# Kernel tuning notes

Measured on AMD Instinct MI355X. Metric: run time of the kernel, lower is better.

Reference implementation:

```python
import jax, jax.numpy as jnp
import numpy as np

NUM_HEADS = 8
EMBED_DIM = 512
EXPAND = 3
RPE_DIM = 512
RPE_LAYERS = 3
B, N = 4, 2048
D1 = (EXPAND * EMBED_DIM) // NUM_HEADS * NUM_HEADS  # 1536
HEAD_DIM = D1 // NUM_HEADS  # 192


def srms(x):
    # SimpleRMSNorm: x / (||x||_2 * d^{-1/2} + eps)
    d = x.shape[-1]
    rms = jnp.linalg.norm(x, axis=-1, keepdims=True) * (d ** -0.5)
    return x / (rms + 1e-8)


def rpe_net(idx, Wp, bp, Wl, bl, Wr, br):
    # idx: (m, 1) relative positions -> (m, h*head_dim)
    h = idx @ Wp.T + bp
    for i in range(Wl.shape[0]):  # fixed small layer count
        h = jax.nn.relu(srms(h)) @ Wl[i].T + bl[i]
    return jax.nn.relu(srms(h)) @ Wr.T + br


def setup_inputs() -> dict:
    key = jax.random.key(0)
    ks = jax.random.split(key, 12)
    s = 0.02
    return {
        "x": jax.random.normal(ks[0], (B, N, EMBED_DIM), jnp.float32),
        "Wu": jax.random.normal(ks[1], (D1, EMBED_DIM), jnp.float32) * s,
        "bu": jnp.zeros((D1,), jnp.float32),
        "Wv": jax.random.normal(ks[2], (D1, EMBED_DIM), jnp.float32) * s,
        "bv": jnp.zeros((D1,), jnp.float32),
        "Wo": jax.random.normal(ks[3], (EMBED_DIM, D1), jnp.float32) * s,
        "bo": jnp.zeros((EMBED_DIM,), jnp.float32),
        "Wp": jax.random.normal(ks[4], (RPE_DIM, 1), jnp.float32) * s,
        "bp": jax.random.normal(ks[5], (RPE_DIM,), jnp.float32) * s,
        "Wl": jax.random.normal(ks[6], (RPE_LAYERS, RPE_DIM, RPE_DIM), jnp.float32) * s,
        "bl": jax.random.normal(ks[7], (RPE_LAYERS, RPE_DIM), jnp.float32) * s,
        "Wr": jax.random.normal(ks[8], (NUM_HEADS * HEAD_DIM, RPE_DIM), jnp.float32) * s,
        "br": jax.random.normal(ks[9], (NUM_HEADS * HEAD_DIM,), jnp.float32) * s,
    }


def reference(x, Wu, bu, Wv, bv, Wo, bo, Wp, bp, Wl, bl, Wr, br):
    b, n, e = x.shape
    d1 = Wu.shape[0]
    hd = d1 // NUM_HEADS
    u = jax.nn.silu(x @ Wu.T + bu)                       # (b, n, d1)
    v = jax.nn.silu(x @ Wv.T + bv)                       # (b, n, d1)
    v = v.reshape(b, n, NUM_HEADS, hd).transpose(0, 2, 1, 3)  # (b, h, n, d)
    # Tno non-causal, par_type=1: indices [0, 1..n-1, 0, -(n-1)..-1]
    pos = jnp.arange(1, n, dtype=x.dtype)
    zero = jnp.zeros((1,), x.dtype)
    idx = jnp.concatenate([zero, pos, zero, -pos[::-1]])[:, None]  # (2n, 1)
    a = rpe_net(idx, Wp, bp, Wl, bl, Wr, br)             # (2n, h*d)
    a = a.reshape(2 * n, NUM_HEADS, hd).transpose(1, 0, 2)  # (h, 2n, d)
    m = 2 * n
    # circular conv of length 2n along sequence, truncate to n
    y = jnp.fft.rfft(v, m, axis=2) * jnp.fft.rfft(a, m, axis=1)[None]
    out = jnp.fft.irfft(y, m, axis=2)[:, :, :n, :]       # (b, h, n, d)
    out = out.transpose(0, 2, 1, 3).reshape(b, n, d1)    # (b, n, d1)
    return (u * out) @ Wo.T + bo
```

## Files before the change

kernel.cpp:

```cpp
#include <hip/hip_runtime.h>

#define N_SEQ 2048
#define M_FFT 4096
#define D1    1536
#define NH    8
#define HD    192
#define ED    512

typedef __bf16 bf16;
typedef __bf16 bf16x2 __attribute__((ext_vector_type(2)));
typedef __bf16 bf16x4 __attribute__((ext_vector_type(4)));
typedef __bf16 bf16x8 __attribute__((ext_vector_type(8)));
typedef float  floatx4 __attribute__((ext_vector_type(4)));

enum { MODE_PLAIN = 0, MODE_SILU_UV = 1, MODE_AT = 3 };

__device__ __forceinline__ void gload16(const void* g, void* l) {
    __builtin_amdgcn_global_load_lds(
        (const __attribute__((address_space(1))) void*)g,
        (__attribute__((address_space(3))) void*)l, 16, 0, 0);
}

template<int MODE, typename OutT>
__global__ __launch_bounds__(256) void gemm_bf16(
    const bf16* __restrict__ A, const bf16* __restrict__ Bw,
    const float* __restrict__ bias, const float* __restrict__ bias2,
    OutT* __restrict__ C, OutT* __restrict__ C2,
    int M, int Nc, int K)
{
    __shared__ __align__(16) bf16 As[128 * 32];
    __shared__ __align__(16) bf16 Bs[128 * 32];

    const int tid  = threadIdx.x;
    const int row0 = blockIdx.y * 128;
    const int col0 = blockIdx.x * 128;
    const int wid  = tid >> 6;
    const int lane = tid & 63;
    const int lm   = lane & 15;
    const int lk   = lane >> 4;
    const int wm   = wid >> 1;
    const int wn   = wid & 1;
    const int ldrow  = tid >> 2;
    const int ldcol8 = (tid & 3) * 8;

    floatx4 acc[4][4] = {};

    const bf16* Ag = A  + ((size_t)(row0 + ldrow)) * K + ldcol8;
    const bf16* Bg = Bw + ((size_t)(col0 + ldrow)) * K + ldcol8;
    bf16* AsW = As + (wid * 16) * 32;
    bf16* BsW = Bs + (wid * 16) * 32;

    for (int k0 = 0; k0 < K; k0 += 32) {
        gload16(Ag + k0, AsW);
        gload16(Ag + (size_t)64 * K + k0, AsW + 64 * 32);
        gload16(Bg + k0, BsW);
        gload16(Bg + (size_t)64 * K + k0, BsW + 64 * 32);
        __syncthreads();

        bf16x8 af[4], bfr[4];
        #pragma unroll
        for (int mi = 0; mi < 4; ++mi)
            af[mi] = *(const bf16x8*)&As[(wm * 64 + mi * 16 + lm) * 32 + lk * 8];
        #pragma unroll
        for (int nj = 0; nj < 4; ++nj)
            bfr[nj] = *(const bf16x8*)&Bs[(wn * 64 + nj * 16 + lm) * 32 + lk * 8];
        #pragma unroll
        for (int mi = 0; mi < 4; ++mi)
            #pragma unroll
            for (int nj = 0; nj < 4; ++nj)
                acc[mi][nj] = __builtin_amdgcn_mfma_f32_16x16x32_bf16(
                    af[mi], bfr[nj], acc[mi][nj], 0, 0, 0);
        __syncthreads();
    }

    const float* bs = bias;
    OutT* dst = C;
    int cadj = 0;
    if (MODE == MODE_SILU_UV && col0 >= D1) { bs = bias2; dst = C2; cadj = D1; }

    float bcol[4];
    #pragma unroll
    for (int nj = 0; nj < 4; ++nj)
        bcol[nj] = bs[col0 - cadj + wn * 64 + nj * 16 + lm];

    #pragma unroll
    for (int mi = 0; mi < 4; ++mi) {
        const int rbase = row0 + wm * 64 + mi * 16 + lk * 4;
        #pragma unroll
        for (int nj = 0; nj < 4; ++nj) {
            const int col = col0 - cadj + wn * 64 + nj * 16 + lm;
            float vals[4];
            #pragma unroll
            for (int r = 0; r < 4; ++r) {
                float val = acc[mi][nj][r] + bcol[nj];
                if (MODE == MODE_SILU_UV)
                    val = val / (1.0f + __expf(-val));
                vals[r] = val;
            }
            if (MODE == MODE_SILU_UV) {
                int b = rbase >> 11, s = rbase & 2047;
                bf16x4 o;
                #pragma unroll
                for (int r = 0; r < 4; ++r) o[r] = (bf16)vals[r];
                *(bf16x4*)&((bf16*)dst)[((size_t)(b * D1 + col)) * N_SEQ + s] = o;
            } else if (MODE == MODE_AT) {
                float4 o = make_float4(vals[0], vals[1], vals[2], vals[3]);
                *(float4*)&((float*)C)[(size_t)col * M + rbase] = o;
            } else {
                #pragma unroll
                for (int r = 0; r < 4; ++r)
                    C[(size_t)(rbase + r) * Nc + col] = (OutT)vals[r];
            }
        }
    }
}

__global__ __launch_bounds__(256) void f2b_all_kernel(
    const float* __restrict__ x,  const float* __restrict__ s0,
    const float* __restrict__ s1, const float* __restrict__ s2,
    const float* __restrict__ s3, const float* __restrict__ s4,
    bf16* __restrict__ x_bf, bf16* __restrict__ w_bf)
{
    const int bid = blockIdx.x;
    const float* src;
    bf16* dst;
    size_t off;
    if (bid < 4096) {
        src = x; dst = x_bf; off = (size_t)bid * 1024;
    } else {
        int t = bid - 4096;
        int seg = t / 768;
        src = seg == 0 ? s0 : seg == 1 ? s1 : seg == 2 ? s2 : seg == 3 ? s3 : s4;
        dst = w_bf + (size_t)seg * 786432;
        off = (size_t)(t % 768) * 1024;
    }
    size_t i = off + (size_t)threadIdx.x * 4;
    float4 f = *(const float4*)(src + i);
    union { bf16 h[4]; short4 s; } u4;
    u4.h[0] = (bf16)f.x; u4.h[1] = (bf16)f.y;
    u4.h[2] = (bf16)f.z; u4.h[3] = (bf16)f.w;
    *(short4*)(dst + i) = u4.s;
}

__global__ __launch_bounds__(256) void rpe_in_srms_kernel(
    const float* __restrict__ Wp, const float* __restrict__ bp,
    bf16* __restrict__ g)
{
    const int j = blockIdx.x;
    const int tid = threadIdx.x;
    float idxv = (j < N_SEQ) ? (float)j
                             : (j == N_SEQ ? 0.0f : (float)(j - 2 * N_SEQ));
    float h1 = idxv * Wp[tid] + bp[tid];
    float h2 = idxv * Wp[tid + 256] + bp[tid + 256];
    float ss = h1 * h1 + h2 * h2;
    #pragma unroll
    for (int off = 32; off > 0; off >>= 1) ss += __shfl_down(ss, off, 64);
    __shared__ float red[4];
    if ((tid & 63) == 0) red[tid >> 6] = ss;
    __syncthreads();
    float tot = red[0] + red[1] + red[2] + red[3];
    float scale = 1.0f / (sqrtf(tot) * 0.04419417382415922f + 1e-8f);
    g[(size_t)j * ED + tid]       = (bf16)fmaxf(h1 * scale, 0.0f);
    g[(size_t)j * ED + tid + 256] = (bf16)fmaxf(h2 * scale, 0.0f);
}

__global__ __launch_bounds__(256) void srms_relu_kernel(
    const float* __restrict__ in, bf16* __restrict__ out)
{
    const int row = blockIdx.x;
    const int tid = threadIdx.x;
    const float* p = in + (size_t)row * ED;

    float ss = 0.0f;
    for (int i = tid; i < ED; i += 256) { float x = p[i]; ss += x * x; }
    #pragma unroll
    for (int off = 32; off > 0; off >>= 1) ss += __shfl_down(ss, off, 64);
    __shared__ float red[4];
    if ((tid & 63) == 0) red[tid >> 6] = ss;
    __syncthreads();
    float tot = red[0] + red[1] + red[2] + red[3];
    float scale = 1.0f / (sqrtf(tot) * 0.04419417382415922f + 1e-8f);
    for (int i = tid; i < ED; i += 256)
        out[(size_t)row * ED + i] = (bf16)fmaxf(p[i] * scale, 0.0f);
}

#define FFT_LDS_SZ 4381
#define CC1 0.9238795325112867f
#define SS1 0.3826834323650898f
#define RR2 0.7071067811865476f

__device__ __forceinline__ int fpad(int i) { return i + (i >> 4) + 2 * (i >> 8); }

__device__ __forceinline__ float2 cmul(float2 a, float2 b) {
    return make_float2(a.x * b.x - a.y * b.y, a.x * b.y + a.y * b.x);
}
__device__ __forceinline__ float2 cadd(float2 a, float2 b) {
    return make_float2(a.x + b.x, a.y + b.y);
}
__device__ __forceinline__ float2 csub(float2 a, float2 b) {
    return make_float2(a.x - b.x, a.y - b.y);
}
__device__ __forceinline__ float2 cneg_i(float2 a) { return make_float2(a.y, -a.x); }
__device__ __forceinline__ float2 cpos_i(float2 a) { return make_float2(-a.y, a.x); }
__host__ __device__ constexpr int brev4(int t) {
    return ((t & 1) << 3) | ((t & 2) << 1) | ((t & 4) >> 1) | ((t & 8) >> 3);
}

template<bool HZ>
__device__ __forceinline__ void fft16_dif_r4(float2 x[16]) {
    const float2 W1 = make_float2( CC1, -SS1);
    const float2 W2 = make_float2( RR2, -RR2);
    const float2 W3 = make_float2( SS1, -CC1);
    const float2 W6 = make_float2(-RR2, -RR2);
    const float2 W9 = make_float2(-CC1,  SS1);
    #pragma unroll
    for (int n = 0; n < 4; ++n) {
        float2 A, B, C, D;
        if (HZ) { A = x[n]; C = x[n]; B = x[n + 4]; D = x[n + 4]; }
        else {
            A = cadd(x[n], x[n + 8]);  C = csub(x[n], x[n + 8]);
            B = cadd(x[n + 4], x[n + 12]); D = csub(x[n + 4], x[n + 12]);
        }
        float2 s = csub(A, B);
        float2 nid = cneg_i(D);
        float2 m = cadd(C, nid);
        float2 p = csub(C, nid);
        x[n] = cadd(A, B);
        if (n == 0)      { x[4] = s;            x[8]  = m;           x[12] = p; }
        else if (n == 1) { x[5] = cmul(s, W2);  x[9]  = cmul(m, W1); x[13] = cmul(p, W3); }
        else if (n == 2) { x[6] = cneg_i(s);    x[10] = cmul(m, W2); x[14] = cmul(p, W6); }
        else             { x[7] = cmul(s, W6);  x[11] = cmul(m, W3); x[15] = cmul(p, W9); }
    }
    #pragma unroll
    for (int q = 0; q < 16; q += 4) {
        float2 a = x[q], b = x[q + 1], c = x[q + 2], d = x[q + 3];
        float2 a1 = cadd(a, c), c1 = csub(a, c);
        float2 b1 = cadd(b, d), d1 = cneg_i(csub(b, d));
        x[q]     = cadd(a1, b1);
        x[q + 1] = csub(a1, b1);
        x[q + 2] = cadd(c1, d1);
        x[q + 3] = csub(c1, d1);
    }
}

template<bool HALF_OUT>
__device__ __forceinline__ void fft16_dit_inv_r4(float2 x[16]) {
    const float2 V1 = make_float2( CC1, SS1);
    const float2 V2 = make_float2( RR2, RR2);
    const float2 V3 = make_float2( SS1, CC1);
    const float2 V6 = make_float2(-RR2, RR2);
    #pragma unroll
    for (int q = 0; q < 16; q += 4) {
        float2 a = x[q], b = x[q + 1], c = x[q + 2], d = x[q + 3];
        float2 a1 = cadd(a, b), b1 = csub(a, b);
        float2 c1 = cadd(c, d), d1 = csub(c, d);
        float2 t = cpos_i(d1);
        x[q]     = cadd(a1, c1);
        x[q + 2] = csub(a1, c1);
        x[q + 1] = cadd(b1, t);
        x[q + 3] = csub(b1, t);
    }
    #pragma unroll
    for (int n = 0; n < 4; ++n) {
        float2 t1, t2;
        if (n == 0)      { t1 = x[4];             t2 = x[12]; }
        else if (n == 1) { t1 = cmul(x[5],  V2);  t2 = cmul(x[13], V2); }
        else if (n == 2) { t1 = cpos_i(x[6]);     t2 = cpos_i(x[14]); }
        else             { t1 = cmul(x[7],  V6);  t2 = cmul(x[15], V6); }
        float2 P = cadd(x[n], t1), Q = csub(x[n], t1);
        float2 R = cadd(x[n + 8], t2), S = csub(x[n + 8], t2);
        float2 t, u;
        if (n == 0)      { t = R;            u = S; }
        else if (n == 1) { t = cmul(R, V1);  u = cmul(S, V1); }
        else if (n == 2) { t = cmul(R, V2);  u = cmul(S, V2); }
        else             { t = cmul(R, V3);  u = cmul(S, V3); }
        float2 iu = cpos_i(u);
        x[n]     = cadd(P, t);
        x[n + 4] = cadd(Q, iu);
        if (!HALF_OUT) {
            x[n + 8]  = csub(P, t);
            x[n + 12] = csub(Q, iu);
        }
    }
}

__device__ __forceinline__ void stage_twiddle_tree(
    float2 v[16], int j, float rden, float sgn)
{
    float s, c;
    __sincosf(sgn * 6.283185307179586f * (float)j * rden, &s, &c);
    float2 w[16];
    w[1] = make_float2(c, s);
    w[2] = cmul(w[1], w[1]);
    w[3] = cmul(w[1], w[2]);
    w[4] = cmul(w[2], w[2]);
    w[5] = cmul(w[1], w[4]);
    w[6] = cmul(w[2], w[4]);
    w[7] = cmul(w[3], w[4]);
    w[8] = cmul(w[4], w[4]);
    #pragma unroll
    for (int t = 9; t < 16; ++t) w[t] = cmul(w[t - 8], w[8]);
    #pragma unroll
    for (int tau = 1; tau < 16; ++tau)
        v[brev4(tau)] = cmul(v[brev4(tau)], w[tau]);
}

template<bool HALF_ZERO>
__device__ void fft4096_fwd(float2* d, int tid)
{
    float2 v[16];
    {
        const int j = tid;
        if (HALF_ZERO) {
            #pragma unroll
            for (int t = 0; t < 8; ++t) v[t] = d[fpad(j + (t << 8))];
            fft16_dif_r4<true>(v);
        } else {
            #pragma unroll
            for (int t = 0; t < 16; ++t) v[t] = d[fpad(j + (t << 8))];
            fft16_dif_r4<false>(v);
        }
        stage_twiddle_tree(v, j, 1.0f / 4096.0f, -1.0f);
        #pragma unroll
        for (int p = 0; p < 16; ++p) d[fpad(j + (p << 8))] = v[p];
    }
    __syncthreads();
    {
        const int base = ((tid >> 4) << 8) + (tid & 15);
        #pragma unroll
        for (int t = 0; t < 16; ++t) v[t] = d[fpad(base + (t << 4))];
        fft16_dif_r4<false>(v);
        stage_twiddle_tree(v, tid & 15, 1.0f / 256.0f, -1.0f);
        #pragma unroll
        for (int p = 0; p < 16; ++p) d[fpad(base + (p << 4))] = v[p];
    }
    __syncthreads();
    {
        const int base = tid << 4;
        #pragma unroll
        for (int t = 0; t < 16; ++t) v[t] = d[fpad(base + t)];
        fft16_dif_r4<false>(v);
        #pragma unroll
        for (int p = 0; p < 16; ++p) d[fpad(base + p)] = v[p];
    }
    __syncthreads();
}

__global__ __launch_bounds__(256) void fft_a_kernel(
    const float* __restrict__ a_t, float2* __restrict__ Wspec)
{
    __shared__ float2 data[FFT_LDS_SZ];
    const int tid = threadIdx.x;
    const int h = blockIdx.x / 96, dp = blockIdx.x % 96;

    const float* r0 = a_t + ((size_t)(h * HD + 2 * dp)) * M_FFT;
    const float* r1 = r0 + M_FFT;

    for (int j = tid; j < 4096; j += 256) data[fpad(j)] = make_float2(r0[j], r1[j]);
    __syncthreads();
    fft4096_fwd<false>(data, tid);

    float2* outrow = Wspec + (size_t)blockIdx.x * 4096;
    for (int j = tid; j < 4096; j += 256) outrow[j] = data[fpad(j)];
}

__global__ __launch_bounds__(256) void fft_conv_kernel(
    const bf16* __restrict__ v_t, const float2* __restrict__ Wspec,
    const bf16* __restrict__ u_t, bf16* __restrict__ gated_t)
{
    __shared__ float2 data[FFT_LDS_SZ];
    const int tid = threadIdx.x;
    const int bx = blockIdx.x;
    const int b  = bx / 768;
    const int r  = bx % 768;
    const int h  = r / 96, dp = r % 96;
    const int ch = h * HD + 2 * dp;

    const bf16* z0 = v_t + ((size_t)(b * D1 + ch)) * N_SEQ;
    const bf16* z1 = z0 + N_SEQ;

    {
        const int s = tid * 8;
        bf16x8 a0 = *(const bf16x8*)(z0 + s);
        bf16x8 a1 = *(const bf16x8*)(z1 + s);
        #pragma unroll
        for (int i = 0; i < 8; ++i)
            data[fpad(s + i)] = make_float2((float)a0[i], (float)a1[i]);
    }
    __syncthreads();

    fft4096_fwd<true>(data, tid);

    const float2* Wrow = Wspec + (size_t)r * 4096;
    float2 v[16];
    {
        const int base = tid << 4;
        #pragma unroll
        for (int i = 0; i < 16; ++i) {
            const int p  = base + i;
            const int k  = __brev((unsigned)p) >> 20;
            const int km = (4096 - k) & 4095;
            const int p2 = __brev((unsigned)km) >> 20;
            float2 Zk = data[fpad(p)];
            float2 Zm = data[fpad(p2)];
            float2 Wk = Wrow[p];
            float2 Wm = Wrow[p2];
            float2 V0 = make_float2(0.5f * (Zk.x + Zm.x), 0.5f * (Zk.y - Zm.y));
            float2 V1 = make_float2(0.5f * (Zk.y + Zm.y), 0.5f * (Zm.x - Zk.x));
            float2 A0 = make_float2(0.5f * (Wk.x + Wm.x), 0.5f * (Wk.y - Wm.y));
            float2 A1 = make_float2(0.5f * (Wk.y + Wm.y), 0.5f * (Wm.x - Wk.x));
            float2 P = cmul(V0, A0), Q = cmul(V1, A1);
            v[i] = make_float2(P.x - Q.y, P.y + Q.x);
        }
        __syncthreads();
        fft16_dit_inv_r4<false>(v);
        #pragma unroll
        for (int i = 0; i < 16; ++i) data[fpad(base + i)] = v[i];
    }
    __syncthreads();
    {
        const int base = ((tid >> 4) << 8) + (tid & 15);
        #pragma unroll
        for (int p = 0; p < 16; ++p) v[p] = data[fpad(base + (p << 4))];
        stage_twiddle_tree(v, tid & 15, 1.0f / 256.0f, 1.0f);
        fft16_dit_inv_r4<false>(v);
        #pragma unroll
        for (int t = 0; t < 16; ++t) data[fpad(base + (t << 4))] = v[t];
    }
    __syncthreads();
    {
        const int j = tid;
        #pragma unroll
        for (int p = 0; p < 16; ++p) v[p] = data[fpad(j + (p << 8))];
        stage_twiddle_tree(v, j, 1.0f / 4096.0f, 1.0f);
        fft16_dit_inv_r4<true>(v);
        #pragma unroll
        for (int t = 0; t < 8; ++t) data[fpad(j + (t << 8))] = v[t];
    }
    __syncthreads();

    const float inv_m = 1.0f / 4096.0f;
    const bf16* u0 = u_t + ((size_t)(b * D1 + ch)) * N_SEQ;
    const bf16* u1 = u0 + N_SEQ;
    bf16* g0 = gated_t + ((size_t)(b * D1 + ch)) * N_SEQ;
    bf16* g1 = g0 + N_SEQ;
    {
        const int t = tid * 8;
        bf16x8 ua = *(const bf16x8*)(u0 + t);
        bf16x8 ub = *(const bf16x8*)(u1 + t);
        bf16x8 oa, ob;
        #pragma unroll
        for (int i = 0; i < 8; ++i) {
            float2 y = data[fpad(t + i)];
            oa[i] = (bf16)(y.x * inv_m * (float)ua[i]);
            ob[i] = (bf16)(y.y * inv_m * (float)ub[i]);
        }
        *(bf16x8*)(g0 + t) = oa;
        *(bf16x8*)(g1 + t) = ob;
    }
}

__global__ __launch_bounds__(256) void transpose_cs_kernel(
    const bf16* __restrict__ in, bf16* __restrict__ outp)
{
    __shared__ bf16 tile[64 * 68];
    const int c0 = blockIdx.x * 64;
    const int m0 = blockIdx.y * 64;
    const int b  = m0 >> 11;
    const int s0 = m0 & 2047;
    const int tid = threadIdx.x;
    const int cl = tid >> 4;
    const int sc = (tid & 15) * 4;
    #pragma unroll
    for (int p = 0; p < 4; ++p) {
        int c = p * 16 + cl;
        bf16x4 v = *(const bf16x4*)&in[((size_t)(b * D1 + c0 + c)) * N_SEQ + s0 + sc];
        *(bf16x4*)&tile[c * 68 + sc] = v;
    }
    __syncthreads();
    const int sl = tid >> 4;
    const int cc = (tid & 15) * 4;
    #pragma unroll
    for (int p = 0; p < 4; ++p) {
        int s = p * 16 + sl;
        bf16x4 o;
        #pragma unroll
        for (int j = 0; j < 4; ++j) o[j] = tile[(cc + j) * 68 + s];
        *(bf16x4*)&outp[((size_t)(m0 + s)) * D1 + c0 + cc] = o;
    }
}

extern "C" void kernel_launch(void* const* d_in, const int* in_sizes, int n_in,
                              void* d_out, int out_size, void* d_ws, size_t ws_size,
                              hipStream_t stream)
{
    const float* x  = (const float*)d_in[0];
    const float* Wu = (const float*)d_in[1];
    const float* bu = (const float*)d_in[2];
    const float* Wv = (const float*)d_in[3];
    const float* bv = (const float*)d_in[4];
    const float* Wo = (const float*)d_in[5];
    const float* bo = (const float*)d_in[6];
    const float* Wp = (const float*)d_in[7];
    const float* bp = (const float*)d_in[8];
    const float* Wl = (const float*)d_in[9];
    const float* bl = (const float*)d_in[10];
    const float* Wr = (const float*)d_in[11];
    const float* br = (const float*)d_in[12];
    float* out = (float*)d_out;

    float* ws      = (float*)d_ws;
    float* a_t     = ws;
    float* Wspec   = a_t   + 6291456;
    float* h0      = Wspec + 6291456;
    bf16*  bfws    = (bf16*)(h0 + 2097152);
    bf16*  x_bf    = bfws;
    bf16*  w_bf    = x_bf    + 4194304;
    bf16*  Wuv_bf  = w_bf;
    bf16*  Wo_bf   = w_bf    + 2 * 786432;
    bf16*  Wl_bf   = Wo_bf   + 786432;
    bf16*  Wr_bf   = Wl_bf   + 786432;
    bf16*  g_bf    = Wr_bf   + 786432;
    bf16*  u_t     = g_bf    + 2097152;
    bf16*  v_t     = u_t     + 12582912;
    bf16*  gated_t = v_t     + 12582912;
    bf16*  gated   = gated_t + 12582912;

    dim3 blk(256);

    f2b_all_kernel<<<4096 + 5 * 768, blk, 0, stream>>>(
        x, Wu, Wv, Wo, Wl, Wr, x_bf, w_bf);

    gemm_bf16<MODE_SILU_UV, bf16><<<dim3(24, 64), blk, 0, stream>>>(
        x_bf, Wuv_bf, bu, bv, u_t, v_t, 8192, 2 * D1, ED);

    rpe_in_srms_kernel<<<4096, blk, 0, stream>>>(Wp, bp, g_bf);
    for (int i = 0; i < 3; ++i) {
        gemm_bf16<MODE_PLAIN, float><<<dim3(4, 32), blk, 0, stream>>>(
            g_bf, Wl_bf + (size_t)i * ED * ED, bl + (size_t)i * ED, nullptr,
            h0, nullptr, 4096, ED, ED);
        srms_relu_kernel<<<4096, blk, 0, stream>>>(h0, g_bf);
    }
    gemm_bf16<MODE_AT, float><<<dim3(12, 32), blk, 0, stream>>>(
        g_bf, Wr_bf, br, nullptr, a_t, nullptr, 4096, D1, ED);

    fft_a_kernel<<<768, blk, 0, stream>>>(a_t, (float2*)Wspec);
    fft_conv_kernel<<<3072, blk, 0, stream>>>(
        v_t, (const float2*)Wspec, u_t, gated_t);

    transpose_cs_kernel<<<dim3(24, 128), blk, 0, stream>>>(gated_t, gated);

    gemm_bf16<MODE_PLAIN, float><<<dim3(4, 64), blk, 0, stream>>>(
        gated, Wo_bf, bo, nullptr, out, nullptr, 8192, ED, D1);
}
```

Before: 365.5 us.

## Fuse RPE SimpleRMSNorm into GEMM epilogues via atomic row sum-of-squares

The standalone srms_relu kernels and the fp32 intermediate h0 are removed. Each RPE layer GEMM now stores relu of the unnormalized output as bf16 and atomically accumulates per-row sums of squares. Since the norm scale is positive, the next GEMM applies it to its accumulators in the epilogue, and the AT GEMM does the same for the last layer. The RPE input kernel and the sumsq zeroing are folded into the f2b conversion launch, and the FFT complex type becomes a float2 ext_vector so the compiler can use packed math. This cuts several launches and an fp32 round trip, at the cost of float atomics and scalar bf16 stores in the epilogue.

Result: no change. 358.8 us (-1.8%).

```diff
diff --git a/kernel.cpp b/kernel.cpp
--- a/kernel.cpp
+++ b/kernel.cpp
@@ -8,12 +8,12 @@
 #define ED    512
 
 typedef __bf16 bf16;
-typedef __bf16 bf16x2 __attribute__((ext_vector_type(2)));
 typedef __bf16 bf16x4 __attribute__((ext_vector_type(4)));
 typedef __bf16 bf16x8 __attribute__((ext_vector_type(8)));
 typedef float  floatx4 __attribute__((ext_vector_type(4)));
-
-enum { MODE_PLAIN = 0, MODE_SILU_UV = 1, MODE_AT = 3 };
+typedef float  cx __attribute__((ext_vector_type(2)));
+
+enum { MODE_PLAIN = 0, MODE_SILU_UV = 1, MODE_AT = 3, MODE_RPE = 4 };
 
 __device__ __forceinline__ void gload16(const void* g, void* l) {
     __builtin_amdgcn_global_load_lds(
@@ -26,7 +26,8 @@
     const bf16* __restrict__ A, const bf16* __restrict__ Bw,
     const float* __restrict__ bias, const float* __restrict__ bias2,
     OutT* __restrict__ C, OutT* __restrict__ C2,
-    int M, int Nc, int K)
+    int M, int Nc, int K,
+    const float* __restrict__ scale_in, float* __restrict__ sumsq_out)
 {
     __shared__ __align__(16) bf16 As[128 * 32];
     __shared__ __align__(16) bf16 Bs[128 * 32];
@@ -83,16 +84,50 @@
     for (int nj = 0; nj < 4; ++nj)
         bcol[nj] = bs[col0 - cadj + wn * 64 + nj * 16 + lm];
 
+    if (MODE == MODE_RPE) {
+        #pragma unroll
+        for (int mi = 0; mi < 4; ++mi) {
+            #pragma unroll
+            for (int r = 0; r < 4; ++r) {
+                const int row = row0 + wm * 64 + mi * 16 + lk * 4 + r;
+                float sc = 1.0f;
+                if (scale_in)
+                    sc = 1.0f / (sqrtf(scale_in[row]) * 0.04419417382415922f + 1e-8f);
+                float ssq = 0.0f;
+                #pragma unroll
+                for (int nj = 0; nj < 4; ++nj) {
+                    const int col = col0 + wn * 64 + nj * 16 + lm;
+                    float val = acc[mi][nj][r] * sc + bcol[nj];
+                    ssq += val * val;
+                    ((bf16*)C)[(size_t)row * Nc + col] = (bf16)fmaxf(val, 0.0f);
+                }
+                ssq += __shfl_xor(ssq, 1, 64);
+                ssq += __shfl_xor(ssq, 2, 64);
+                ssq += __shfl_xor(ssq, 4, 64);
+                ssq += __shfl_xor(ssq, 8, 64);
+                if (lm == 0) atomicAdd(&sumsq_out[row], ssq);
+            }
+        }
+        return;
+    }
+
     #pragma unroll
     for (int mi = 0; mi < 4; ++mi) {
         const int rbase = row0 + wm * 64 + mi * 16 + lk * 4;
+        float sc[4];
+        #pragma unroll
+        for (int r = 0; r < 4; ++r) {
+            sc[r] = 1.0f;
+            if (MODE == MODE_AT && scale_in)
+                sc[r] = 1.0f / (sqrtf(scale_in[rbase + r]) * 0.04419417382415922f + 1e-8f);
+        }
         #pragma unroll
         for (int nj = 0; nj < 4; ++nj) {
             const int col = col0 - cadj + wn * 64 + nj * 16 + lm;
             float vals[4];
             #pragma unroll
             for (int r = 0; r < 4; ++r) {
-                float val = acc[mi][nj][r] + bcol[nj];
+                float val = acc[mi][nj][r] * sc[r] + bcol[nj];
                 if (MODE == MODE_SILU_UV)
                     val = val / (1.0f + __expf(-val));
                 vals[r] = val;
@@ -119,69 +154,53 @@
     const float* __restrict__ x,  const float* __restrict__ s0,
     const float* __restrict__ s1, const float* __restrict__ s2,
     const float* __restrict__ s3, const float* __restrict__ s4,
-    bf16* __restrict__ x_bf, bf16* __restrict__ w_bf)
+    const float* __restrict__ Wp, const float* __restrict__ bp,
+    bf16* __restrict__ x_bf, bf16* __restrict__ w_bf,
+    float* __restrict__ sumsq, bf16* __restrict__ g0)
 {
     const int bid = blockIdx.x;
-    const float* src;
-    bf16* dst;
-    size_t off;
-    if (bid < 4096) {
-        src = x; dst = x_bf; off = (size_t)bid * 1024;
+    const int tid = threadIdx.x;
+    __shared__ float red[4];
+
+    if (bid < 7936) {
+        const float* src;
+        bf16* dst;
+        size_t off;
+        if (bid < 4096) {
+            src = x; dst = x_bf; off = (size_t)bid * 1024;
+        } else {
+            int t = bid - 4096;
+            int seg = t / 768;
+            src = seg == 0 ? s0 : seg == 1 ? s1 : seg == 2 ? s2
+                : seg == 3 ? s3 : s4;
+            dst = w_bf + (size_t)seg * 786432;
+            off = (size_t)(t % 768) * 1024;
+        }
+        size_t i = off + (size_t)tid * 4;
+        float4 f = *(const float4*)(src + i);
+        union { bf16 h[4]; short4 s; } u4;
+        u4.h[0] = (bf16)f.x; u4.h[1] = (bf16)f.y;
+        u4.h[2] = (bf16)f.z; u4.h[3] = (bf16)f.w;
+        *(short4*)(dst + i) = u4.s;
+    } else if (bid < 7948) {
+        size_t i = (size_t)(bid - 7936) * 1024 + (size_t)tid * 4;
+        *(float4*)(sumsq + i) = make_float4(0.f, 0.f, 0.f, 0.f);
     } else {
-        int t = bid - 4096;
-        int seg = t / 768;
-        src = seg == 0 ? s0 : seg == 1 ? s1 : seg == 2 ? s2 : seg == 3 ? s3 : s4;
-        dst = w_bf + (size_t)seg * 786432;
-        off = (size_t)(t % 768) * 1024;
-    }
-    size_t i = off + (size_t)threadIdx.x * 4;
-    float4 f = *(const float4*)(src + i);
-    union { bf16 h[4]; short4 s; } u4;
-    u4.h[0] = (bf16)f.x; u4.h[1] = (bf16)f.y;
-    u4.h[2] = (bf16)f.z; u4.h[3] = (bf16)f.w;
-    *(short4*)(dst + i) = u4.s;
-}
-
-__global__ __launch_bounds__(256) void rpe_in_srms_kernel(
-    const float* __restrict__ Wp, const float* __restrict__ bp,
-    bf16* __restrict__ g)
-{
-    const int j = blockIdx.x;
-    const int tid = threadIdx.x;
-    float idxv = (j < N_SEQ) ? (float)j
-                             : (j == N_SEQ ? 0.0f : (float)(j - 2 * N_SEQ));
-    float h1 = idxv * Wp[tid] + bp[tid];
-    float h2 = idxv * Wp[tid + 256] + bp[tid + 256];
-    float ss = h1 * h1 + h2 * h2;
-    #pragma unroll
-    for (int off = 32; off > 0; off >>= 1) ss += __shfl_down(ss, off, 64);
-    __shared__ float red[4];
-    if ((tid & 63) == 0) red[tid >> 6] = ss;
-    __syncthreads();
-    float tot = red[0] + red[1] + red[2] + red[3];
-    float scale = 1.0f / (sqrtf(tot) * 0.04419417382415922f + 1e-8f);
-    g[(size_t)j * ED + tid]       = (bf16)fmaxf(h1 * scale, 0.0f);
-    g[(size_t)j * ED + tid + 256] = (bf16)fmaxf(h2 * scale, 0.0f);
-}
-
-__global__ __launch_bounds__(256) void srms_relu_kernel(
-    const float* __restrict__ in, bf16* __restrict__ out)
-{
-    const int row = blockIdx.x;
-    const int tid = threadIdx.x;
-    const float* p = in + (size_t)row * ED;
-
-    float ss = 0.0f;
-    for (int i = tid; i < ED; i += 256) { float x = p[i]; ss += x * x; }
-    #pragma unroll
-    for (int off = 32; off > 0; off >>= 1) ss += __shfl_down(ss, off, 64);
-    __shared__ float red[4];
-    if ((tid & 63) == 0) red[tid >> 6] = ss;
-    __syncthreads();
-    float tot = red[0] + red[1] + red[2] + red[3];
-    float scale = 1.0f / (sqrtf(tot) * 0.04419417382415922f + 1e-8f);
-    for (int i = tid; i < ED; i += 256)
-        out[(size_t)row * ED + i] = (bf16)fmaxf(p[i] * scale, 0.0f);
+        const int j = bid - 7948;
+        float idxv = (j < N_SEQ) ? (float)j
+                                 : (j == N_SEQ ? 0.0f : (float)(j - 2 * N_SEQ));
+        float h1 = idxv * Wp[tid] + bp[tid];
+        float h2 = idxv * Wp[tid + 256] + bp[tid + 256];
+        float ss = h1 * h1 + h2 * h2;
+        #pragma unroll
+        for (int off = 32; off > 0; off >>= 1) ss += __shfl_down(ss, off, 64);
+        if ((tid & 63) == 0) red[tid >> 6] = ss;
+        __syncthreads();
+        float tot = red[0] + red[1] + red[2] + red[3];
+        float scale = 1.0f / (sqrtf(tot) * 0.04419417382415922f + 1e-8f);
+        g0[(size_t)j * ED + tid]       = (bf16)fmaxf(h1 * scale, 0.0f);
+        g0[(size_t)j * ED + tid + 256] = (bf16)fmaxf(h2 * scale, 0.0f);
+    }
 }
 
 #define FFT_LDS_SZ 4381
@@ -191,41 +210,37 @@
 
 __device__ __forceinline__ int fpad(int i) { return i + (i >> 4) + 2 * (i >> 8); }
 
-__device__ __forceinline__ float2 cmul(float2 a, float2 b) {
-    return make_float2(a.x * b.x - a.y * b.y, a.x * b.y + a.y * b.x);
-}
-__device__ __forceinline__ float2 cadd(float2 a, float2 b) {
-    return make_float2(a.x + b.x, a.y + b.y);
-}
-__device__ __forceinline__ float2 csub(float2 a, float2 b) {
-    return make_float2(a.x - b.x, a.y - b.y);
-}
-__device__ __forceinline__ float2 cneg_i(float2 a) { return make_float2(a.y, -a.x); }
-__device__ __forceinline__ float2 cpos_i(float2 a) { return make_float2(-a.y, a.x); }
+__device__ __forceinline__ cx mkcx(float a, float b) { cx r; r.x = a; r.y = b; return r; }
+__device__ __forceinline__ cx cmul(cx a, cx b) {
+    cx br = mkcx(-b.y, b.x);
+    return a.xx * b + a.yy * br;
+}
+__device__ __forceinline__ cx cneg_i(cx a) { return mkcx(a.y, -a.x); }
+__device__ __forceinline__ cx cpos_i(cx a) { return mkcx(-a.y, a.x); }
 __host__ __device__ constexpr int brev4(int t) {
     return ((t & 1) << 3) | ((t & 2) << 1) | ((t & 4) >> 1) | ((t & 8) >> 3);
 }
 
 template<bool HZ>
-__device__ __forceinline__ void fft16_dif_r4(float2 x[16]) {
-    const float2 W1 = make_float2( CC1, -SS1);
-    const float2 W2 = make_float2( RR2, -RR2);
-    const float2 W3 = make_float2( SS1, -CC1);
-    const float2 W6 = make_float2(-RR2, -RR2);
-    const float2 W9 = make_float2(-CC1,  SS1);
+__device__ __forceinline__ void fft16_dif_r4(cx x[16]) {
+    const cx W1 = mkcx( CC1, -SS1);
+    const cx W2 = mkcx( RR2, -RR2);
+    const cx W3 = mkcx( SS1, -CC1);
+    const cx W6 = mkcx(-RR2, -RR2);
+    const cx W9 = mkcx(-CC1,  SS1);
     #pragma unroll
     for (int n = 0; n < 4; ++n) {
-        float2 A, B, C, D;
+        cx A, B, C, D;
         if (HZ) { A = x[n]; C = x[n]; B = x[n + 4]; D = x[n + 4]; }
         else {
-            A = cadd(x[n], x[n + 8]);  C = csub(x[n], x[n + 8]);
-            B = cadd(x[n + 4], x[n + 12]); D = csub(x[n + 4], x[n + 12]);
-        }
-        float2 s = csub(A, B);
-        float2 nid = cneg_i(D);
-        float2 m = cadd(C, nid);
-        float2 p = csub(C, nid);
-        x[n] = cadd(A, B);
+            A = x[n] + x[n + 8];      C = x[n] - x[n + 8];
+            B = x[n + 4] + x[n + 12]; D = x[n + 4] - x[n + 12];
+        }
+        cx s = A - B;
+        cx nid = cneg_i(D);
+        cx m = C + nid;
+        cx p = C - nid;
+        x[n] = A + B;
         if (n == 0)      { x[4] = s;            x[8]  = m;           x[12] = p; }
         else if (n == 1) { x[5] = cmul(s, W2);  x[9]  = cmul(m, W1); x[13] = cmul(p, W3); }
         else if (n == 2) { x[6] = cneg_i(s);    x[10] = cmul(m, W2); x[14] = cmul(p, W6); }
@@ -233,64 +248,64 @@
     }
     #pragma unroll
     for (int q = 0; q < 16; q += 4) {
-        float2 a = x[q], b = x[q + 1], c = x[q + 2], d = x[q + 3];
-        float2 a1 = cadd(a, c), c1 = csub(a, c);
-        float2 b1 = cadd(b, d), d1 = cneg_i(csub(b, d));
-        x[q]     = cadd(a1, b1);
-        x[q + 1] = csub(a1, b1);
-        x[q + 2] = cadd(c1, d1);
-        x[q + 3] = csub(c1, d1);
+        cx a = x[q], b = x[q + 1], c = x[q + 2], d = x[q + 3];
+        cx a1 = a + c, c1 = a - c;
+        cx b1 = b + d, d1 = cneg_i(b - d);
+        x[q]     = a1 + b1;
+        x[q + 1] = a1 - b1;
+        x[q + 2] = c1 + d1;
+        x[q + 3] = c1 - d1;
     }
 }
 
 template<bool HALF_OUT>
-__device__ __forceinline__ void fft16_dit_inv_r4(float2 x[16]) {
-    const float2 V1 = make_float2( CC1, SS1);
-    const float2 V2 = make_float2( RR2, RR2);
-    const float2 V3 = make_float2( SS1, CC1);
-    const float2 V6 = make_float2(-RR2, RR2);
+__device__ __forceinline__ void fft16_dit_inv_r4(cx x[16]) {
+    const cx V1 = mkcx( CC1, SS1);
+    const cx V2 = mkcx( RR2, RR2);
+    const cx V3 = mkcx( SS1, CC1);
+    const cx V6 = mkcx(-RR2, RR2);
     #pragma unroll
     for (int q = 0; q < 16; q += 4) {
-        float2 a = x[q], b = x[q + 1], c = x[q + 2], d = x[q + 3];
-        float2 a1 = cadd(a, b), b1 = csub(a, b);
-        float2 c1 = cadd(c, d), d1 = csub(c, d);
-        float2 t = cpos_i(d1);
-        x[q]     = cadd(a1, c1);
-        x[q + 2] = csub(a1, c1);
-        x[q + 1] = cadd(b1, t);
-        x[q + 3] = csub(b1, t);
+        cx a = x[q], b = x[q + 1], c = x[q + 2], d = x[q + 3];
+        cx a1 = a + b, b1 = a - b;
+        cx c1 = c + d, d1 = c - d;
+        cx t = cpos_i(d1);
+        x[q]     = a1 + c1;
+        x[q + 2] = a1 - c1;
+        x[q + 1] = b1 + t;
+        x[q + 3] = b1 - t;
     }
     #pragma unroll
     for (int n = 0; n < 4; ++n) {
-        float2 t1, t2;
+        cx t1, t2;
         if (n == 0)      { t1 = x[4];             t2 = x[12]; }
         else if (n == 1) { t1 = cmul(x[5],  V2);  t2 = cmul(x[13], V2); }
         else if (n == 2) { t1 = cpos_i(x[6]);     t2 = cpos_i(x[14]); }
         else             { t1 = cmul(x[7],  V6);  t2 = cmul(x[15], V6); }
-        float2 P = cadd(x[n], t1), Q = csub(x[n], t1);
-        float2 R = cadd(x[n + 8], t2), S = csub(x[n + 8], t2);
-        float2 t, u;
+        cx P = x[n] + t1, Q = x[n] - t1;
+        cx R = x[n + 8] + t2, S = x[n + 8] - t2;
+        cx t, u;
         if (n == 0)      { t = R;            u = S; }
         else if (n == 1) { t = cmul(R, V1);  u = cmul(S, V1); }
         else if (n == 2) { t = cmul(R, V2);  u = cmul(S, V2); }
         else             { t = cmul(R, V3);  u = cmul(S, V3); }
-        float2 iu = cpos_i(u);
-        x[n]     = cadd(P, t);
-        x[n + 4] = cadd(Q, iu);
+        cx iu = cpos_i(u);
+        x[n]     = P + t;
+        x[n + 4] = Q + iu;
         if (!HALF_OUT) {
-            x[n + 8]  = csub(P, t);
-            x[n + 12] = csub(Q, iu);
+            x[n + 8]  = P - t;
+            x[n + 12] = Q - iu;
         }
     }
 }
 
 __device__ __forceinline__ void stage_twiddle_tree(
-    float2 v[16], int j, float rden, float sgn)
+    cx v[16], int j, float rden, float sgn)
 {
     float s, c;
     __sincosf(sgn * 6.283185307179586f * (float)j * rden, &s, &c);
-    float2 w[16];
-    w[1] = make_float2(c, s);
+    cx w[16];
+    w[1] = mkcx(c, s);
     w[2] = cmul(w[1], w[1]);
     w[3] = cmul(w[1], w[2]);
     w[4] = cmul(w[2], w[2]);
@@ -306,9 +321,9 @@
 }
 
 template<bool HALF_ZERO>
-__device__ void fft4096_fwd(float2* d, int tid)
-{
-    float2 v[16];
+__device__ void fft4096_fwd(cx* d, int tid)
+{
+    cx v[16];
     {
         const int j = tid;
         if (HALF_ZERO) {
@@ -347,28 +362,28 @@
 }
 
 __global__ __launch_bounds__(256) void fft_a_kernel(
-    const float* __restrict__ a_t, float2* __restrict__ Wspec)
-{
-    __shared__ float2 data[FFT_LDS_SZ];
+    const float* __restrict__ a_t, cx* __restrict__ Wspec)
+{
+    __shared__ cx data[FFT_LDS_SZ];
     const int tid = threadIdx.x;
     const int h = blockIdx.x / 96, dp = blockIdx.x % 96;
 
     const float* r0 = a_t + ((size_t)(h * HD + 2 * dp)) * M_FFT;
     const float* r1 = r0 + M_FFT;
 
-    for (int j = tid; j < 4096; j += 256) data[fpad(j)] = make_float2(r0[j], r1[j]);
+    for (int j = tid; j < 4096; j += 256) data[fpad(j)] = mkcx(r0[j], r1[j]);
     __syncthreads();
     fft4096_fwd<false>(data, tid);
 
-    float2* outrow = Wspec + (size_t)blockIdx.x * 4096;
+    cx* outrow = Wspec + (size_t)blockIdx.x * 4096;
     for (int j = tid; j < 4096; j += 256) outrow[j] = data[fpad(j)];
 }
 
 __global__ __launch_bounds__(256) void fft_conv_kernel(
-    const bf16* __restrict__ v_t, const float2* __restrict__ Wspec,
+    const bf16* __restrict__ v_t, const cx* __restrict__ Wspec,
     const bf16* __restrict__ u_t, bf16* __restrict__ gated_t)
 {
-    __shared__ float2 data[FFT_LDS_SZ];
+    __shared__ cx data[FFT_LDS_SZ];
     const int tid = threadIdx.x;
     const int bx = blockIdx.x;
     const int b  = bx / 768;
@@ -385,14 +400,14 @@
         bf16x8 a1 = *(const bf16x8*)(z1 + s);
         #pragma unroll
         for (int i = 0; i < 8; ++i)
-            data[fpad(s + i)] = make_float2((float)a0[i], (float)a1[i]);
+            data[fpad(s + i)] = mkcx((float)a0[i], (float)a1[i]);
     }
     __syncthreads();
 
     fft4096_fwd<true>(data, tid);
 
-    const float2* Wrow = Wspec + (size_t)r * 4096;
-    float2 v[16];
+    const cx* Wrow = Wspec + (size_t)r * 4096;
+    cx v[16];
     {
         const int base = tid << 4;
         #pragma unroll
@@ -401,16 +416,16 @@
             const int k  = __brev((unsigned)p) >> 20;
             const int km = (4096 - k) & 4095;
             const int p2 = __brev((unsigned)km) >> 20;
-            float2 Zk = data[fpad(p)];
-            float2 Zm = data[fpad(p2)];
-            float2 Wk = Wrow[p];
-            float2 Wm = Wrow[p2];
-            float2 V0 = make_float2(0.5f * (Zk.x + Zm.x), 0.5f * (Zk.y - Zm.y));
-            float2 V1 = make_float2(0.5f * (Zk.y + Zm.y), 0.5f * (Zm.x - Zk.x));
-            float2 A0 = make_float2(0.5f * (Wk.x + Wm.x), 0.5f * (Wk.y - Wm.y));
-            float2 A1 = make_float2(0.5f * (Wk.y + Wm.y), 0.5f * (Wm.x - Wk.x));
-            float2 P = cmul(V0, A0), Q = cmul(V1, A1);
-            v[i] = make_float2(P.x - Q.y, P.y + Q.x);
+            cx Zk = data[fpad(p)];
+            cx Zm = data[fpad(p2)];
+            cx Wk = Wrow[p];
+            cx Wm = Wrow[p2];
+            cx V0 = 0.5f * (Zk + mkcx(Zm.x, -Zm.y));
+            cx V1 = 0.5f * (mkcx(Zk.y, -Zk.x) + mkcx(Zm.y, Zm.x));
+            cx A0 = 0.5f * (Wk + mkcx(Wm.x, -Wm.y));
+            cx A1 = 0.5f * (mkcx(Wk.y, -Wk.x) + mkcx(Wm.y, Wm.x));
+            cx P = cmul(V0, A0), Q = cmul(V1, A1);
+            v[i] = P + cpos_i(Q);
         }
         __syncthreads();
         fft16_dit_inv_r4<false>(v);
@@ -451,7 +466,7 @@
         bf16x8 oa, ob;
         #pragma unroll
         for (int i = 0; i < 8; ++i) {
-            float2 y = data[fpad(t + i)];
+            cx y = data[fpad(t + i)];
             oa[i] = (bf16)(y.x * inv_m * (float)ua[i]);
             ob[i] = (bf16)(y.y * inv_m * (float)ub[i]);
         }
@@ -512,44 +527,49 @@
     float* ws      = (float*)d_ws;
     float* a_t     = ws;
     float* Wspec   = a_t   + 6291456;
-    float* h0      = Wspec + 6291456;
-    bf16*  bfws    = (bf16*)(h0 + 2097152);
+    float* sumsq   = Wspec + 6291456;
+    bf16*  bfws    = (bf16*)(sumsq + 12288);
     bf16*  x_bf    = bfws;
     bf16*  w_bf    = x_bf    + 4194304;
     bf16*  Wuv_bf  = w_bf;
     bf16*  Wo_bf   = w_bf    + 2 * 786432;
     bf16*  Wl_bf   = Wo_bf   + 786432;
     bf16*  Wr_bf   = Wl_bf   + 786432;
-    bf16*  g_bf    = Wr_bf   + 786432;
-    bf16*  u_t     = g_bf    + 2097152;
+    bf16*  gA      = Wr_bf   + 786432;
+    bf16*  gB      = gA      + 2097152;
+    bf16*  u_t     = gB      + 2097152;
     bf16*  v_t     = u_t     + 12582912;
     bf16*  gated_t = v_t     + 12582912;
     bf16*  gated   = gated_t + 12582912;
 
     dim3 blk(256);
 
-    f2b_all_kernel<<<4096 + 5 * 768, blk, 0, stream>>>(
-        x, Wu, Wv, Wo, Wl, Wr, x_bf, w_bf);
+    f2b_all_kernel<<<4096 + 5 * 768 + 12 + 4096, blk, 0, stream>>>(
+        x, Wu, Wv, Wo, Wl, Wr, Wp, bp, x_bf, w_bf, sumsq, gA);
 
     gemm_bf16<MODE_SILU_UV, bf16><<<dim3(24, 64), blk, 0, stream>>>(
-        x_bf, Wuv_bf, bu, bv, u_t, v_t, 8192, 2 * D1, ED);
-
-    rpe_in_srms_kernel<<<4096, blk, 0, stream>>>(Wp, bp, g_bf);
+        x_bf, Wuv_bf, bu, bv, u_t, v_t, 8192, 2 * D1, ED, nullptr, nullptr);
+
+    bf16* gin = gA;
+    bf16* gout = gB;
     for (int i = 0; i < 3; ++i) {
-        gemm_bf16<MODE_PLAIN, float><<<dim3(4, 32), blk, 0, stream>>>(
-            g_bf, Wl_bf + (size_t)i * ED * ED, bl + (size_t)i * ED, nullptr,
-            h0, nullptr, 4096, ED, ED);
-        srms_relu_kernel<<<4096, blk, 0, stream>>>(h0, g_bf);
+        const float* sin_p = (i == 0) ? nullptr : sumsq + (size_t)(i - 1) * 4096;
+        gemm_bf16<MODE_RPE, bf16><<<dim3(4, 32), blk, 0, stream>>>(
+            gin, Wl_bf + (size_t)i * ED * ED, bl + (size_t)i * ED, nullptr,
+            gout, nullptr, 4096, ED, ED, sin_p, sumsq + (size_t)i * 4096);
+        bf16* t = gin; gin = gout; gout = t;
     }
     gemm_bf16<MODE_AT, float><<<dim3(12, 32), blk, 0, stream>>>(
-        g_bf, Wr_bf, br, nullptr, a_t, nullptr, 4096, D1, ED);
-
-    fft_a_kernel<<<768, blk, 0, stream>>>(a_t, (float2*)Wspec);
+        gin, Wr_bf, br, nullptr, a_t, nullptr, 4096, D1, ED,
+        sumsq + 2 * 4096, nullptr);
+
+    fft_a_kernel<<<768, blk, 0, stream>>>(a_t, (cx*)Wspec);
     fft_conv_kernel<<<3072, blk, 0, stream>>>(
-        v_t, (const float2*)Wspec, u_t, gated_t);
+        v_t, (const cx*)Wspec, u_t, gated_t);
 
     transpose_cs_kernel<<<dim3(24, 128), blk, 0, stream>>>(gated_t, gated);
 
     gemm_bf16<MODE_PLAIN, float><<<dim3(4, 64), blk, 0, stream>>>(
-        gated, Wo_bf, bo, nullptr, out, nullptr, 8192, ED, D1);
-}
+        gated, Wo_bf, bo, nullptr, out, nullptr, 8192, ED, D1,
+        nullptr, nullptr);
+}
```

## Fuse SimpleRMSNorm+ReLU into RPE GEMM epilogues via deferred per-row scaling

Applied to the files above, without the earlier changes.

Removes the separate srms_relu kernels and the fp32 h0 intermediate. Each RPE GEMM epilogue now writes relu(h) directly as bf16 and atomically accumulates per-row sum of squares. The following GEMM applies the row-wise RMS scale to its accumulator, which is valid because a positive per-row scale commutes with ReLU and with the matmul. The initial RPE srms kernel is folded into the fp32-to-bf16 conversion launch, which also zeroes the sumsq buffer. This cuts several launches and a float round trip through memory, at the cost of atomics and of storing unnormalized activations in bf16.

Result: no change. 362.3 us, median of 2 (-0.9%).

```diff
diff --git a/kernel.cpp b/kernel.cpp
--- a/kernel.cpp
+++ b/kernel.cpp
@@ -8,12 +8,11 @@
 #define ED    512
 
 typedef __bf16 bf16;
-typedef __bf16 bf16x2 __attribute__((ext_vector_type(2)));
 typedef __bf16 bf16x4 __attribute__((ext_vector_type(4)));
 typedef __bf16 bf16x8 __attribute__((ext_vector_type(8)));
 typedef float  floatx4 __attribute__((ext_vector_type(4)));
 
-enum { MODE_PLAIN = 0, MODE_SILU_UV = 1, MODE_AT = 3 };
+enum { MODE_PLAIN = 0, MODE_SILU_UV = 1, MODE_AT = 3, MODE_RPE = 4 };
 
 __device__ __forceinline__ void gload16(const void* g, void* l) {
     __builtin_amdgcn_global_load_lds(
@@ -26,7 +25,8 @@
     const bf16* __restrict__ A, const bf16* __restrict__ Bw,
     const float* __restrict__ bias, const float* __restrict__ bias2,
     OutT* __restrict__ C, OutT* __restrict__ C2,
-    int M, int Nc, int K)
+    int M, int Nc, int K,
+    const float* __restrict__ scale_in, float* __restrict__ sumsq_out)
 {
     __shared__ __align__(16) bf16 As[128 * 32];
     __shared__ __align__(16) bf16 Bs[128 * 32];
@@ -83,16 +83,50 @@
     for (int nj = 0; nj < 4; ++nj)
         bcol[nj] = bs[col0 - cadj + wn * 64 + nj * 16 + lm];
 
+    if (MODE == MODE_RPE) {
+        #pragma unroll
+        for (int mi = 0; mi < 4; ++mi) {
+            #pragma unroll
+            for (int r = 0; r < 4; ++r) {
+                const int row = row0 + wm * 64 + mi * 16 + lk * 4 + r;
+                float sc = 1.0f;
+                if (scale_in)
+                    sc = 1.0f / (sqrtf(scale_in[row]) * 0.04419417382415922f + 1e-8f);
+                float ssq = 0.0f;
+                #pragma unroll
+                for (int nj = 0; nj < 4; ++nj) {
+                    const int col = col0 + wn * 64 + nj * 16 + lm;
+                    float val = acc[mi][nj][r] * sc + bcol[nj];
+                    ssq += val * val;
+                    ((bf16*)C)[(size_t)row * Nc + col] = (bf16)fmaxf(val, 0.0f);
+                }
+                ssq += __shfl_xor(ssq, 1, 64);
+                ssq += __shfl_xor(ssq, 2, 64);
+                ssq += __shfl_xor(ssq, 4, 64);
+                ssq += __shfl_xor(ssq, 8, 64);
+                if (lm == 0) atomicAdd(&sumsq_out[row], ssq);
+            }
+        }
+        return;
+    }
+
     #pragma unroll
     for (int mi = 0; mi < 4; ++mi) {
         const int rbase = row0 + wm * 64 + mi * 16 + lk * 4;
+        float sc[4];
+        #pragma unroll
+        for (int r = 0; r < 4; ++r) {
+            sc[r] = 1.0f;
+            if (MODE == MODE_AT && scale_in)
+                sc[r] = 1.0f / (sqrtf(scale_in[rbase + r]) * 0.04419417382415922f + 1e-8f);
+        }
         #pragma unroll
         for (int nj = 0; nj < 4; ++nj) {
             const int col = col0 - cadj + wn * 64 + nj * 16 + lm;
             float vals[4];
             #pragma unroll
             for (int r = 0; r < 4; ++r) {
-                float val = acc[mi][nj][r] + bcol[nj];
+                float val = acc[mi][nj][r] * sc[r] + bcol[nj];
                 if (MODE == MODE_SILU_UV)
                     val = val / (1.0f + __expf(-val));
                 vals[r] = val;
@@ -119,69 +153,53 @@
     const float* __restrict__ x,  const float* __restrict__ s0,
     const float* __restrict__ s1, const float* __restrict__ s2,
     const float* __restrict__ s3, const float* __restrict__ s4,
-    bf16* __restrict__ x_bf, bf16* __restrict__ w_bf)
+    const float* __restrict__ Wp, const float* __restrict__ bp,
+    bf16* __restrict__ x_bf, bf16* __restrict__ w_bf,
+    float* __restrict__ sumsq, bf16* __restrict__ g0)
 {
     const int bid = blockIdx.x;
-    const float* src;
-    bf16* dst;
-    size_t off;
-    if (bid < 4096) {
-        src = x; dst = x_bf; off = (size_t)bid * 1024;
+    const int tid = threadIdx.x;
+    __shared__ float red[4];
+
+    if (bid < 7936) {
+        const float* src;
+        bf16* dst;
+        size_t off;
+        if (bid < 4096) {
+            src = x; dst = x_bf; off = (size_t)bid * 1024;
+        } else {
+            int t = bid - 4096;
+            int seg = t / 768;
+            src = seg == 0 ? s0 : seg == 1 ? s1 : seg == 2 ? s2
+                : seg == 3 ? s3 : s4;
+            dst = w_bf + (size_t)seg * 786432;
+            off = (size_t)(t % 768) * 1024;
+        }
+        size_t i = off + (size_t)tid * 4;
+        float4 f = *(const float4*)(src + i);
+        union { bf16 h[4]; short4 s; } u4;
+        u4.h[0] = (bf16)f.x; u4.h[1] = (bf16)f.y;
+        u4.h[2] = (bf16)f.z; u4.h[3] = (bf16)f.w;
+        *(short4*)(dst + i) = u4.s;
+    } else if (bid < 7948) {
+        size_t i = (size_t)(bid - 7936) * 1024 + (size_t)tid * 4;
+        *(float4*)(sumsq + i) = make_float4(0.f, 0.f, 0.f, 0.f);
     } else {
-        int t = bid - 4096;
-        int seg = t / 768;
-        src = seg == 0 ? s0 : seg == 1 ? s1 : seg == 2 ? s2 : seg == 3 ? s3 : s4;
-        dst = w_bf + (size_t)seg * 786432;
-        off = (size_t)(t % 768) * 1024;
-    }
-    size_t i = off + (size_t)threadIdx.x * 4;
-    float4 f = *(const float4*)(src + i);
-    union { bf16 h[4]; short4 s; } u4;
-    u4.h[0] = (bf16)f.x; u4.h[1] = (bf16)f.y;
-    u4.h[2] = (bf16)f.z; u4.h[3] = (bf16)f.w;
-    *(short4*)(dst + i) = u4.s;
-}
-
-__global__ __launch_bounds__(256) void rpe_in_srms_kernel(
-    const float* __restrict__ Wp, const float* __restrict__ bp,
-    bf16* __restrict__ g)
-{
-    const int j = blockIdx.x;
-    const int tid = threadIdx.x;
-    float idxv = (j < N_SEQ) ? (float)j
-                             : (j == N_SEQ ? 0.0f : (float)(j - 2 * N_SEQ));
-    float h1 = idxv * Wp[tid] + bp[tid];
-    float h2 = idxv * Wp[tid + 256] + bp[tid + 256];
-    float ss = h1 * h1 + h2 * h2;
-    #pragma unroll
-    for (int off = 32; off > 0; off >>= 1) ss += __shfl_down(ss, off, 64);
-    __shared__ float red[4];
-    if ((tid & 63) == 0) red[tid >> 6] = ss;
-    __syncthreads();
-    float tot = red[0] + red[1] + red[2] + red[3];
-    float scale = 1.0f / (sqrtf(tot) * 0.04419417382415922f + 1e-8f);
-    g[(size_t)j * ED + tid]       = (bf16)fmaxf(h1 * scale, 0.0f);
-    g[(size_t)j * ED + tid + 256] = (bf16)fmaxf(h2 * scale, 0.0f);
-}
-
-__global__ __launch_bounds__(256) void srms_relu_kernel(
-    const float* __restrict__ in, bf16* __restrict__ out)
-{
-    const int row = blockIdx.x;
-    const int tid = threadIdx.x;
-    const float* p = in + (size_t)row * ED;
-
-    float ss = 0.0f;
-    for (int i = tid; i < ED; i += 256) { float x = p[i]; ss += x * x; }
-    #pragma unroll
-    for (int off = 32; off > 0; off >>= 1) ss += __shfl_down(ss, off, 64);
-    __shared__ float red[4];
-    if ((tid & 63) == 0) red[tid >> 6] = ss;
-    __syncthreads();
-    float tot = red[0] + red[1] + red[2] + red[3];
-    float scale = 1.0f / (sqrtf(tot) * 0.04419417382415922f + 1e-8f);
-    for (int i = tid; i < ED; i += 256)
-        out[(size_t)row * ED + i] = (bf16)fmaxf(p[i] * scale, 0.0f);
+        const int j = bid - 7948;
+        float idxv = (j < N_SEQ) ? (float)j
+                                 : (j == N_SEQ ? 0.0f : (float)(j - 2 * N_SEQ));
+        float h1 = idxv * Wp[tid] + bp[tid];
+        float h2 = idxv * Wp[tid + 256] + bp[tid + 256];
+        float ss = h1 * h1 + h2 * h2;
+        #pragma unroll
+        for (int off = 32; off > 0; off >>= 1) ss += __shfl_down(ss, off, 64);
+        if ((tid & 63) == 0) red[tid >> 6] = ss;
+        __syncthreads();
+        float tot = red[0] + red[1] + red[2] + red[3];
+        float scale = 1.0f / (sqrtf(tot) * 0.04419417382415922f + 1e-8f);
+        g0[(size_t)j * ED + tid]       = (bf16)fmaxf(h1 * scale, 0.0f);
+        g0[(size_t)j * ED + tid + 256] = (bf16)fmaxf(h2 * scale, 0.0f);
+    }
 }
 
 #define FFT_LDS_SZ 4381
@@ -512,37 +530,41 @@
     float* ws      = (float*)d_ws;
     float* a_t     = ws;
     float* Wspec   = a_t   + 6291456;
-    float* h0      = Wspec + 6291456;
-    bf16*  bfws    = (bf16*)(h0 + 2097152);
+    float* sumsq   = Wspec + 6291456;
+    bf16*  bfws    = (bf16*)(sumsq + 12288);
     bf16*  x_bf    = bfws;
     bf16*  w_bf    = x_bf    + 4194304;
     bf16*  Wuv_bf  = w_bf;
     bf16*  Wo_bf   = w_bf    + 2 * 786432;
     bf16*  Wl_bf   = Wo_bf   + 786432;
     bf16*  Wr_bf   = Wl_bf   + 786432;
-    bf16*  g_bf    = Wr_bf   + 786432;
-    bf16*  u_t     = g_bf    + 2097152;
+    bf16*  gA      = Wr_bf   + 786432;
+    bf16*  gB      = gA      + 2097152;
+    bf16*  u_t     = gB      + 2097152;
     bf16*  v_t     = u_t     + 12582912;
     bf16*  gated_t = v_t     + 12582912;
     bf16*  gated   = gated_t + 12582912;
 
     dim3 blk(256);
 
-    f2b_all_kernel<<<4096 + 5 * 768, blk, 0, stream>>>(
-        x, Wu, Wv, Wo, Wl, Wr, x_bf, w_bf);
+    f2b_all_kernel<<<4096 + 5 * 768 + 12 + 4096, blk, 0, stream>>>(
+        x, Wu, Wv, Wo, Wl, Wr, Wp, bp, x_bf, w_bf, sumsq, gA);
 
     gemm_bf16<MODE_SILU_UV, bf16><<<dim3(24, 64), blk, 0, stream>>>(
-        x_bf, Wuv_bf, bu, bv, u_t, v_t, 8192, 2 * D1, ED);
-
-    rpe_in_srms_kernel<<<4096, blk, 0, stream>>>(Wp, bp, g_bf);
+        x_bf, Wuv_bf, bu, bv, u_t, v_t, 8192, 2 * D1, ED, nullptr, nullptr);
+
+    bf16* gin = gA;
+    bf16* gout = gB;
     for (int i = 0; i < 3; ++i) {
-        gemm_bf16<MODE_PLAIN, float><<<dim3(4, 32), blk, 0, stream>>>(
-            g_bf, Wl_bf + (size_t)i * ED * ED, bl + (size_t)i * ED, nullptr,
-            h0, nullptr, 4096, ED, ED);
-        srms_relu_kernel<<<4096, blk, 0, stream>>>(h0, g_bf);
+        const float* sin_p = (i == 0) ? nullptr : sumsq + (size_t)(i - 1) * 4096;
+        gemm_bf16<MODE_RPE, bf16><<<dim3(4, 32), blk, 0, stream>>>(
+            gin, Wl_bf + (size_t)i * ED * ED, bl + (size_t)i * ED, nullptr,
+            gout, nullptr, 4096, ED, ED, sin_p, sumsq + (size_t)i * 4096);
+        bf16* t = gin; gin = gout; gout = t;
     }
     gemm_bf16<MODE_AT, float><<<dim3(12, 32), blk, 0, stream>>>(
-        g_bf, Wr_bf, br, nullptr, a_t, nullptr, 4096, D1, ED);
+        gin, Wr_bf, br, nullptr, a_t, nullptr, 4096, D1, ED,
+        sumsq + 2 * 4096, nullptr);
 
     fft_a_kernel<<<768, blk, 0, stream>>>(a_t, (float2*)Wspec);
     fft_conv_kernel<<<3072, blk, 0, stream>>>(
@@ -551,5 +573,6 @@
     transpose_cs_kernel<<<dim3(24, 128), blk, 0, stream>>>(gated_t, gated);
 
     gemm_bf16<MODE_PLAIN, float><<<dim3(4, 64), blk, 0, stream>>>(
-        gated, Wo_bf, bo, nullptr, out, nullptr, 8192, ED, D1);
-}
+        gated, Wo_bf, bo, nullptr, out, nullptr, 8192, ED, D1,
+        nullptr, nullptr);
+}
```
